# Kernel optimization log

Hardware: AMD Instinct MI355X
Metric: run time of the kernel (lower is better)

## Reference

```python
import jax, jax.numpy as jnp
import numpy as np

N_MODELS = 64
IN_F = 256
OUT_F = 256
BATCH = 8192


def setup_inputs() -> dict:
    key = jax.random.key(0)
    kx, kw, kb, ki = jax.random.split(key, 4)
    x = jax.random.normal(kx, (BATCH, OUT_F), dtype=jnp.float32)
    idxs = jax.random.randint(ki, (BATCH,), 0, N_MODELS, dtype=jnp.int64)
    # learned parameters (torch inits them to zeros; we use random so grads/outputs are nontrivial)
    w = jax.random.normal(kw, (N_MODELS, IN_F, OUT_F), dtype=jnp.float32) * 0.02
    b = jax.random.normal(kb, (N_MODELS, OUT_F), dtype=jnp.float32) * 0.02
    return {"x": x, "idxs": idxs, "w": w, "b": b}


def reference(x, idxs, w, b):
    # torch: baddbmm(b[idxs,:,None], w[idxs], x[:,:,None]).squeeze(-1) -> relu
    # y[n, i] = b[idxs[n], i] + sum_o w[idxs[n], i, o] * x[n, o]
    wg = w[idxs]                      # (B, in, out) gathered per-sample weights
    bg = b[idxs]                      # (B, out)
    y = jnp.einsum('bio,bo->bi', wg, x) + bg
    return jax.nn.relu(y)
```

## Files before the change

### kernel.cpp

```cpp
#include <hip/hip_runtime.h>
#include <stdint.h>


#define N_MODELS 64
#define IN_F     256
#define OUT_F    256
#define BATCH    8192
#define BM       128
#define BN       128
#define PK       264

typedef __bf16 bf16x8 __attribute__((ext_vector_type(8)));
typedef float  f32x4  __attribute__((ext_vector_type(4)));

__device__ __forceinline__ bf16x8 pack8(float4 a, float4 b) {
  bf16x8 o;
  o[0] = (__bf16)a.x; o[1] = (__bf16)a.y; o[2] = (__bf16)a.z; o[3] = (__bf16)a.w;
  o[4] = (__bf16)b.x; o[5] = (__bf16)b.y; o[6] = (__bf16)b.z; o[7] = (__bf16)b.w;
  return o;
}

__global__ __launch_bounds__(256) void fused_kernel(
    const float* __restrict__ x, const int* __restrict__ idxs,
    const float* __restrict__ w, const float* __restrict__ bias_g,
    float* __restrict__ out) {
  const int model = blockIdx.x >> 2;
  const int tile  = (blockIdx.x >> 1) & 1;
  const int i0    = (blockIdx.x & 1) * BN;
  const int t     = threadIdx.x;
  const int lane  = t & 63;
  const int wv    = t >> 6;

  __shared__ unsigned short a_lds[BM][PK];
  __shared__ unsigned short b_lds[BN][PK];
  __shared__ int rid[BM];
  __shared__ int wsum[4];

  const int rw = t >> 1;
  const int h  = t & 1;

  const int4* ip = (const int4*)idxs + t * 8;
  int4 iv[8];
#pragma unroll
  for (int j = 0; j < 8; ++j) iv[j] = ip[j];

  const float* wrow = w + (size_t)model * (IN_F * OUT_F)
                        + (size_t)(i0 + rw) * IN_F + h * 128;
  if (tile == 0) {
#pragma unroll
    for (int j = 0; j < 16; ++j) {
      float4 a = *(const float4*)(wrow + j * 8);
      float4 b = *(const float4*)(wrow + j * 8 + 4);
      *(bf16x8*)&b_lds[rw][h * 128 + j * 8] = pack8(a, b);
    }
  }

  if (t < BM) rid[t] = -1;

  int cnt = 0;
#pragma unroll
  for (int j = 0; j < 8; ++j) {
    int4 v = iv[j];
    cnt += (v.x == model) + (v.y == model) + (v.z == model) + (v.w == model);
  }
  int inc = cnt;
#pragma unroll
  for (int d = 1; d < 64; d <<= 1) {
    int u = __shfl_up(inc, d);
    if (lane >= d) inc += u;
  }
  if (lane == 63) wsum[wv] = inc;
  __syncthreads();
  int wpre = 0, total = 0;
#pragma unroll
  for (int j = 0; j < 4; ++j) {
    int s = wsum[j];
    total += s;
    if (j < wv) wpre += s;
  }
  const int start = tile * BM;
  if (start >= total) return;
  int off = wpre + inc - cnt - start;
#pragma unroll
  for (int j = 0; j < 8; ++j) {
    int4 v = iv[j];
    int n0 = t * 32 + j * 4;
    if (v.x == model) { if ((unsigned)off < BM) rid[off] = n0 + 0; ++off; }
    if (v.y == model) { if ((unsigned)off < BM) rid[off] = n0 + 1; ++off; }
    if (v.z == model) { if ((unsigned)off < BM) rid[off] = n0 + 2; ++off; }
    if (v.w == model) { if ((unsigned)off < BM) rid[off] = n0 + 3; ++off; }
  }
  __syncthreads();

  if (tile == 1) {
#pragma unroll
    for (int j = 0; j < 16; ++j) {
      float4 a = *(const float4*)(wrow + j * 8);
      float4 b = *(const float4*)(wrow + j * 8 + 4);
      *(bf16x8*)&b_lds[rw][h * 128 + j * 8] = pack8(a, b);
    }
  }

  const int srow = rid[rw];
  const float* xrow = x + (size_t)(srow < 0 ? 0 : srow) * IN_F + h * 128;
#pragma unroll
  for (int j = 0; j < 16; ++j) {
    float4 a = *(const float4*)(xrow + j * 8);
    float4 b = *(const float4*)(xrow + j * 8 + 4);
    *(bf16x8*)&a_lds[rw][h * 128 + j * 8] = pack8(a, b);
  }

  const int wm   = (wv & 1) * 64;
  const int wn   = (wv >> 1) * 64;
  const int col  = lane & 15;
  const int quad = lane >> 4;
  float bv[4];
  const float* bp = bias_g + model * OUT_F + i0 + wn + col;
#pragma unroll
  for (int nt = 0; nt < 4; ++nt) bv[nt] = bp[nt * 16];

  __syncthreads();

  f32x4 acc[4][4];
#pragma unroll
  for (int mt = 0; mt < 4; ++mt)
#pragma unroll
    for (int nt = 0; nt < 4; ++nt)
      acc[mt][nt] = (f32x4){bv[nt], bv[nt], bv[nt], bv[nt]};

#pragma unroll
  for (int ks = 0; ks < 8; ++ks) {
    bf16x8 af[4], bfr[4];
#pragma unroll
    for (int mt = 0; mt < 4; ++mt)
      af[mt] = *(const bf16x8*)&a_lds[wm + mt * 16 + col][ks * 32 + quad * 8];
#pragma unroll
    for (int nt = 0; nt < 4; ++nt)
      bfr[nt] = *(const bf16x8*)&b_lds[wn + nt * 16 + col][ks * 32 + quad * 8];
#pragma unroll
    for (int mt = 0; mt < 4; ++mt)
#pragma unroll
      for (int nt = 0; nt < 4; ++nt)
        acc[mt][nt] = __builtin_amdgcn_mfma_f32_16x16x32_bf16(
            af[mt], bfr[nt], acc[mt][nt], 0, 0, 0);
  }

#pragma unroll
  for (int mt = 0; mt < 4; ++mt) {
#pragma unroll
    for (int reg = 0; reg < 4; ++reg) {
      const int mm = wm + mt * 16 + quad * 4 + reg;
      const int s = rid[mm];
      if (s >= 0) {
        float* orow = out + (size_t)s * OUT_F + i0 + wn + col;
#pragma unroll
        for (int nt = 0; nt < 4; ++nt)
          orow[nt * 16] = fmaxf(acc[mt][nt][reg], 0.0f);
      }
    }
  }
}

extern "C" void kernel_launch(void* const* d_in, const int* in_sizes, int n_in,
                              void* d_out, int out_size, void* d_ws, size_t ws_size,
                              hipStream_t stream) {
  const float* x    = (const float*)d_in[0];
  const int*   idxs = (const int*)d_in[1];
  const float* w    = (const float*)d_in[2];
  const float* b    = (const float*)d_in[3];
  float* out = (float*)d_out;
  (void)d_ws; (void)ws_size;

  fused_kernel<<<N_MODELS * 4, 256, 0, stream>>>(x, idxs, w, b, out);
}
```

Baseline: 88.72 us.

## Quadruple block size to 16 waves with 32x32 MFMA tiles per wave

Each block now runs 1024 threads instead of 256, so 16 waves share the 128x128 output tile and each wave computes a 32x32 sub-tile. Staging is split the same way: each thread loads a quarter as much of x, w and the index array. The launch was one lightly occupied block per CU, so the aim is more outstanding global loads and more waves to hide load latency. In exchange, each wave reuses each LDS fragment across fewer MFMAs, and the prefix scan and barriers now span more waves.

```diff
diff --git a/kernel.cpp b/kernel.cpp
--- a/kernel.cpp
+++ b/kernel.cpp
@@ -20,7 +20,7 @@
   return o;
 }
 
-__global__ __launch_bounds__(256) void fused_kernel(
+__global__ __launch_bounds__(1024) void fused_kernel(
     const float* __restrict__ x, const int* __restrict__ idxs,
     const float* __restrict__ w, const float* __restrict__ bias_g,
     float* __restrict__ out) {
@@ -34,35 +34,30 @@
   __shared__ unsigned short a_lds[BM][PK];
   __shared__ unsigned short b_lds[BN][PK];
   __shared__ int rid[BM];
-  __shared__ int wsum[4];
+  __shared__ int wsum[16];
 
-  const int rw = t >> 1;
-  const int h  = t & 1;
+  const int rw = t >> 3;
+  const int h  = t & 7;
 
-  const int4* ip = (const int4*)idxs + t * 8;
-  int4 iv[8];
-#pragma unroll
-  for (int j = 0; j < 8; ++j) iv[j] = ip[j];
+  const int4* ip = (const int4*)idxs + t * 2;
+  int4 iv0 = ip[0], iv1 = ip[1];
 
   const float* wrow = w + (size_t)model * (IN_F * OUT_F)
-                        + (size_t)(i0 + rw) * IN_F + h * 128;
+                        + (size_t)(i0 + rw) * IN_F + h * 32;
+
   if (tile == 0) {
+    float4 tw[8];
 #pragma unroll
-    for (int j = 0; j < 16; ++j) {
-      float4 a = *(const float4*)(wrow + j * 8);
-      float4 b = *(const float4*)(wrow + j * 8 + 4);
-      *(bf16x8*)&b_lds[rw][h * 128 + j * 8] = pack8(a, b);
-    }
+    for (int j = 0; j < 8; ++j) tw[j] = *(const float4*)(wrow + j * 4);
+#pragma unroll
+    for (int j = 0; j < 4; ++j)
+      *(bf16x8*)&b_lds[rw][h * 32 + j * 8] = pack8(tw[2 * j], tw[2 * j + 1]);
   }
 
   if (t < BM) rid[t] = -1;
 
-  int cnt = 0;
-#pragma unroll
-  for (int j = 0; j < 8; ++j) {
-    int4 v = iv[j];
-    cnt += (v.x == model) + (v.y == model) + (v.z == model) + (v.w == model);
-  }
+  int cnt = (iv0.x == model) + (iv0.y == model) + (iv0.z == model) + (iv0.w == model)
+          + (iv1.x == model) + (iv1.y == model) + (iv1.z == model) + (iv1.w == model);
   int inc = cnt;
 #pragma unroll
   for (int d = 1; d < 64; d <<= 1) {
@@ -73,7 +68,7 @@
   __syncthreads();
   int wpre = 0, total = 0;
 #pragma unroll
-  for (int j = 0; j < 4; ++j) {
+  for (int j = 0; j < 16; ++j) {
     int s = wsum[j];
     total += s;
     if (j < wv) wpre += s;
@@ -81,72 +76,76 @@
   const int start = tile * BM;
   if (start >= total) return;
   int off = wpre + inc - cnt - start;
-#pragma unroll
-  for (int j = 0; j < 8; ++j) {
-    int4 v = iv[j];
-    int n0 = t * 32 + j * 4;
-    if (v.x == model) { if ((unsigned)off < BM) rid[off] = n0 + 0; ++off; }
-    if (v.y == model) { if ((unsigned)off < BM) rid[off] = n0 + 1; ++off; }
-    if (v.z == model) { if ((unsigned)off < BM) rid[off] = n0 + 2; ++off; }
-    if (v.w == model) { if ((unsigned)off < BM) rid[off] = n0 + 3; ++off; }
+  {
+    int n0 = t * 8;
+    if (iv0.x == model) { if ((unsigned)off < BM) rid[off] = n0 + 0; ++off; }
+    if (iv0.y == model) { if ((unsigned)off < BM) rid[off] = n0 + 1; ++off; }
+    if (iv0.z == model) { if ((unsigned)off < BM) rid[off] = n0 + 2; ++off; }
+    if (iv0.w == model) { if ((unsigned)off < BM) rid[off] = n0 + 3; ++off; }
+    if (iv1.x == model) { if ((unsigned)off < BM) rid[off] = n0 + 4; ++off; }
+    if (iv1.y == model) { if ((unsigned)off < BM) rid[off] = n0 + 5; ++off; }
+    if (iv1.z == model) { if ((unsigned)off < BM) rid[off] = n0 + 6; ++off; }
+    if (iv1.w == model) { if ((unsigned)off < BM) rid[off] = n0 + 7; ++off; }
   }
   __syncthreads();
 
   if (tile == 1) {
+    float4 tw[8];
 #pragma unroll
-    for (int j = 0; j < 16; ++j) {
-      float4 a = *(const float4*)(wrow + j * 8);
-      float4 b = *(const float4*)(wrow + j * 8 + 4);
-      *(bf16x8*)&b_lds[rw][h * 128 + j * 8] = pack8(a, b);
-    }
+    for (int j = 0; j < 8; ++j) tw[j] = *(const float4*)(wrow + j * 4);
+#pragma unroll
+    for (int j = 0; j < 4; ++j)
+      *(bf16x8*)&b_lds[rw][h * 32 + j * 8] = pack8(tw[2 * j], tw[2 * j + 1]);
   }
 
   const int srow = rid[rw];
-  const float* xrow = x + (size_t)(srow < 0 ? 0 : srow) * IN_F + h * 128;
+  const float* xrow = x + (size_t)(srow < 0 ? 0 : srow) * IN_F + h * 32;
+  {
+    float4 tx[8];
 #pragma unroll
-  for (int j = 0; j < 16; ++j) {
-    float4 a = *(const float4*)(xrow + j * 8);
-    float4 b = *(const float4*)(xrow + j * 8 + 4);
-    *(bf16x8*)&a_lds[rw][h * 128 + j * 8] = pack8(a, b);
+    for (int j = 0; j < 8; ++j) tx[j] = *(const float4*)(xrow + j * 4);
+#pragma unroll
+    for (int j = 0; j < 4; ++j)
+      *(bf16x8*)&a_lds[rw][h * 32 + j * 8] = pack8(tx[2 * j], tx[2 * j + 1]);
   }
 
-  const int wm   = (wv & 1) * 64;
-  const int wn   = (wv >> 1) * 64;
+  const int wm   = (wv & 3) * 32;
+  const int wn   = (wv >> 2) * 32;
   const int col  = lane & 15;
   const int quad = lane >> 4;
-  float bv[4];
+  float bv[2];
   const float* bp = bias_g + model * OUT_F + i0 + wn + col;
 #pragma unroll
-  for (int nt = 0; nt < 4; ++nt) bv[nt] = bp[nt * 16];
+  for (int nt = 0; nt < 2; ++nt) bv[nt] = bp[nt * 16];
 
   __syncthreads();
 
-  f32x4 acc[4][4];
+  f32x4 acc[2][2];
 #pragma unroll
-  for (int mt = 0; mt < 4; ++mt)
+  for (int mt = 0; mt < 2; ++mt)
 #pragma unroll
-    for (int nt = 0; nt < 4; ++nt)
+    for (int nt = 0; nt < 2; ++nt)
       acc[mt][nt] = (f32x4){bv[nt], bv[nt], bv[nt], bv[nt]};
 
 #pragma unroll
   for (int ks = 0; ks < 8; ++ks) {
-    bf16x8 af[4], bfr[4];
+    bf16x8 af[2], bfr[2];
 #pragma unroll
-    for (int mt = 0; mt < 4; ++mt)
+    for (int mt = 0; mt < 2; ++mt)
       af[mt] = *(const bf16x8*)&a_lds[wm + mt * 16 + col][ks * 32 + quad * 8];
 #pragma unroll
-    for (int nt = 0; nt < 4; ++nt)
+    for (int nt = 0; nt < 2; ++nt)
       bfr[nt] = *(const bf16x8*)&b_lds[wn + nt * 16 + col][ks * 32 + quad * 8];
 #pragma unroll
-    for (int mt = 0; mt < 4; ++mt)
+    for (int mt = 0; mt < 2; ++mt)
 #pragma unroll
-      for (int nt = 0; nt < 4; ++nt)
+      for (int nt = 0; nt < 2; ++nt)
         acc[mt][nt] = __builtin_amdgcn_mfma_f32_16x16x32_bf16(
             af[mt], bfr[nt], acc[mt][nt], 0, 0, 0);
   }
 
 #pragma unroll
-  for (int mt = 0; mt < 4; ++mt) {
+  for (int mt = 0; mt < 2; ++mt) {
 #pragma unroll
     for (int reg = 0; reg < 4; ++reg) {
       const int mm = wm + mt * 16 + quad * 4 + reg;
@@ -154,7 +153,7 @@
       if (s >= 0) {
         float* orow = out + (size_t)s * OUT_F + i0 + wn + col;
 #pragma unroll
-        for (int nt = 0; nt < 4; ++nt)
+        for (int nt = 0; nt < 2; ++nt)
           orow[nt * 16] = fmaxf(acc[mt][nt][reg], 0.0f);
       }
     }
@@ -171,5 +170,5 @@
   float* out = (float*)d_out;
   (void)d_ws; (void)ws_size;
 
-  fused_kernel<<<N_MODELS * 4, 256, 0, stream>>>(x, idxs, w, b, out);
+  fused_kernel<<<N_MODELS * 4, 1024, 0, stream>>>(x, idxs, w, b, out);
 }
```

New measurement: 85.77 us. 3.3% less time.
